# Optimization experiments

Hardware: AMD Instinct MI355X
Metric: run time of the kernel (lower is better)

Reference implementation:

```python
import jax, jax.numpy as jnp
import numpy as np

B, N, C, H = 1, 256, 128, 4
DH = C // H  # per-head dim = 32
KEY_SCALE = DH ** -0.5


def setup_inputs() -> dict:
    key = jax.random.key(0)
    ks = jax.random.split(key, 9)
    return {
        "q_data": jax.random.normal(ks[0], (B, N, N, C), jnp.float32),
        "m_data": jax.random.normal(ks[1], (B, N, N, C), jnp.float32),
        "bias": jax.random.normal(ks[2], (B, N, 1, 1, N), jnp.float32),
        "nonbatched_bias": jax.random.normal(ks[3], (1, H, N, N), jnp.float32),
        "wq": jax.random.normal(ks[4], (C, C), jnp.float32) * (1.0 / np.sqrt(C)),
        "wk": jax.random.normal(ks[5], (C, C), jnp.float32) * (1.0 / np.sqrt(C)),
        "wv": jax.random.normal(ks[6], (C, C), jnp.float32) * (1.0 / np.sqrt(C)),
        "wo": jax.random.normal(ks[7], (C, C), jnp.float32) * (1.0 / np.sqrt(C)),
        "bo": jnp.zeros((C,), jnp.float32),
        "wg": jax.random.normal(ks[8], (C, C), jnp.float32) * (1.0 / np.sqrt(C)),
        "bg": jnp.ones((C,), jnp.float32),
    }


def reference(q_data, m_data, bias, nonbatched_bias, wq, wk, wv, wo, bo, wg, bg):
    # projections (torch Linear: x @ W.T), weights stored [out, in]
    q = (q_data @ wq.T) * KEY_SCALE            # [B, N, Nq, H*DH]
    k = m_data @ wk.T                          # [B, N, Nk, H*DH]
    v = m_data @ wv.T                          # [B, N, Nk, H*DH]
    q = q.reshape(B, N, N, H, DH)
    k = k.reshape(B, N, N, H, DH)
    v = v.reshape(B, N, N, H, DH)
    # logits: [B, N, H, Nq, Nk]
    logits = jnp.einsum("bnqhd,bnkhd->bnhqk", q, k)
    logits = logits + bias + nonbatched_bias   # bias [B,N,1,1,Nk]; nb [1,H,Nq,Nk]
    weight = jax.nn.softmax(logits, axis=-1)
    wa = jnp.einsum("bnhqk,bnkhd->bnqhd", weight, v)  # [B, N, Nq, H, DH]
    g = jax.nn.sigmoid(q_data @ wg.T + bg).reshape(B, N, N, H, DH)
    wa = wa * g
    out = wa.reshape(B, N, N, H * DH) @ wo.T + bo
    return out
```

## Files before the change

### kernel.cpp

```cpp
#include <hip/hip_runtime.h>
#include <hip/hip_bf16.h>

typedef unsigned short u16;
typedef unsigned int u32;

#define N_ 256
#define C_ 128
#define H_ 4
#define DH_ 32
#define R_ (N_*N_)

static constexpr float KEY_SCALE_ = 0.17677669529663687f;

typedef __attribute__((ext_vector_type(8))) short bf16x8;
typedef __attribute__((ext_vector_type(4))) float f32x4;

__device__ __forceinline__ float bf2f(u16 b){ return __uint_as_float(((u32)b)<<16); }
__device__ __forceinline__ u16 f2bf(float f){
  u32 u = __float_as_uint(f);
  u += 0x7FFFu + ((u>>16)&1u);
  return (u16)(u>>16);
}

__global__ __launch_bounds__(256) void wconv_kernel(
    const float* __restrict__ wq, const float* __restrict__ wk,
    const float* __restrict__ wv, const float* __restrict__ wg,
    u16* __restrict__ wtb)
{
  int id = blockIdx.x*256 + threadIdx.x;
  int m = id >> 12;
  int e = (id & 4095)*4;
  const float* src = (m==0) ? wq : (m==1) ? wk : (m==2) ? wv : wg;
  const float4 v = *(const float4*)(src + e);
  const float s = (m==0) ? KEY_SCALE_ : 1.f;
  ushort4 o;
  o.x = f2bf(v.x*s); o.y = f2bf(v.y*s); o.z = f2bf(v.z*s); o.w = f2bf(v.w*s);
  *(ushort4*)(wtb + m*16384 + e) = o;
}

#define XSTR 136
__global__ __launch_bounds__(256, 2) void proj_kernel(
    const float* __restrict__ qd, const float* __restrict__ md,
    const u16* __restrict__ wtb, const float* __restrict__ bg,
    u16* __restrict__ qb, u16* __restrict__ kb,
    u16* __restrict__ vb, u16* __restrict__ gb)
{
  __shared__ u16 Xs[256*XSTR];
  const int t = threadIdx.x;
  const int y = blockIdx.y;
  const size_t row0 = (size_t)blockIdx.x * 256;
  const float* X = y ? md : qd;

  #pragma unroll
  for (int p=0;p<16;p++){
    int id = t + p*256;
    int r = id >> 4, c0 = (id & 15)*8;
    const float* s = X + (row0 + r)*C_ + c0;
    float4 a = *(const float4*)s;
    float4 b = *(const float4*)(s+4);
    u16* d = &Xs[r*XSTR + c0];
    d[0]=f2bf(a.x); d[1]=f2bf(a.y); d[2]=f2bf(a.z); d[3]=f2bf(a.w);
    d[4]=f2bf(b.x); d[5]=f2bf(b.y); d[6]=f2bf(b.z); d[7]=f2bf(b.w);
  }

  const int w = t >> 6, l = t & 63, c = l & 15, g = l >> 4;
  const int matSel = w >> 1;
  const int ctBase = (w & 1) * 4;
  const int matIdx = y ? (matSel ? 2 : 1) : (matSel ? 3 : 0);
  u16* dst = y ? (matSel ? vb : kb) : (matSel ? gb : qb);
  const bool doSig = (!y) && matSel;

  bf16x8 bfr[4][4];
  {
    const u16* wb = wtb + matIdx*16384;
    #pragma unroll
    for (int ctj=0;ctj<4;ctj++){
      const u16* rp = wb + ((ctBase+ctj)*16 + c)*C_ + g*8;
      #pragma unroll
      for (int kk=0;kk<4;kk++)
        bfr[ctj][kk] = *(const bf16x8*)(rp + kk*32);
    }
  }
  float bgv[4];
  if (doSig){
    #pragma unroll
    for (int ctj=0;ctj<4;ctj++) bgv[ctj] = bg[(ctBase+ctj)*16 + c];
  }
  __syncthreads();

  for (int mt=0; mt<16; mt++){
    bf16x8 af[4];
    #pragma unroll
    for (int kk=0;kk<4;kk++)
      af[kk] = *(const bf16x8*)&Xs[(mt*16 + c)*XSTR + kk*32 + g*8];
    f32x4 a0 = {0.f,0.f,0.f,0.f}, a1 = {0.f,0.f,0.f,0.f};
    f32x4 a2 = {0.f,0.f,0.f,0.f}, a3 = {0.f,0.f,0.f,0.f};
    #pragma unroll
    for (int kk=0;kk<4;kk++){
      a0 = __builtin_amdgcn_mfma_f32_16x16x32_bf16(af[kk], bfr[0][kk], a0, 0,0,0);
      a1 = __builtin_amdgcn_mfma_f32_16x16x32_bf16(af[kk], bfr[1][kk], a1, 0,0,0);
      a2 = __builtin_amdgcn_mfma_f32_16x16x32_bf16(af[kk], bfr[2][kk], a2, 0,0,0);
      a3 = __builtin_amdgcn_mfma_f32_16x16x32_bf16(af[kk], bfr[3][kk], a3, 0,0,0);
    }
    f32x4 accs[4] = {a0,a1,a2,a3};
    #pragma unroll
    for (int ctj=0;ctj<4;ctj++){
      #pragma unroll
      for (int r=0;r<4;r++){
        float v = accs[ctj][r];
        if (doSig) v = 1.f/(1.f+__expf(-(v + bgv[ctj])));
        dst[(row0 + mt*16 + 4*g + r)*C_ + (ctBase+ctj)*16 + c] = f2bf(v);
      }
    }
  }
}

#define VSTR 264
__global__ __launch_bounds__(256) void attn_kernel(
    const u16* qb, const u16* __restrict__ kb,
    const u16* __restrict__ vb, const u16* __restrict__ gb,
    const float* __restrict__ bias, const float* __restrict__ nbias,
    u16* wab)
{
  __shared__ u16 Vt[32*VSTR];
  __shared__ u16 Ps[4][16][VSTR];
  __shared__ float Bs[256];

  const int t  = threadIdx.x;
  const int h  = blockIdx.x;
  const int n  = blockIdx.y;
  const int w  = t >> 6;
  const int l  = t & 63;
  const int c  = l & 15;
  const int g  = l >> 4;

  {
    const u16* vsrc = vb + ((size_t)n*N_)*C_ + h*DH_;
    for (int id = t; id < 1024; id += 256){
      int k = id >> 2, ch = id & 3;
      ushort4 a = *(const ushort4*)(vsrc + (size_t)k*C_ + ch*8);
      ushort4 b = *(const ushort4*)(vsrc + (size_t)k*C_ + ch*8 + 4);
      int d0 = ch*8;
      Vt[(d0+0)*VSTR + k] = a.x;  Vt[(d0+1)*VSTR + k] = a.y;
      Vt[(d0+2)*VSTR + k] = a.z;  Vt[(d0+3)*VSTR + k] = a.w;
      Vt[(d0+4)*VSTR + k] = b.x;  Vt[(d0+5)*VSTR + k] = b.y;
      Vt[(d0+6)*VSTR + k] = b.z;  Vt[(d0+7)*VSTR + k] = b.w;
    }
    Bs[t] = bias[(size_t)n*N_ + t];
  }
  __syncthreads();

  bf16x8 kf[16];
  {
    const u16* kbase = kb + ((size_t)(n*N_ + c))*C_ + h*DH_ + g*8;
    #pragma unroll
    for (int kt=0;kt<16;kt++)
      kf[kt] = *(const bf16x8*)(kbase + (size_t)kt*16*C_);
  }

  const float* nbp = nbias + (size_t)h*N_*N_;

  for (int qt=0; qt<4; qt++){
    const int q0 = w*64 + qt*16;

    bf16x8 af = *(const bf16x8*)(qb + ((size_t)(n*N_ + q0 + c))*C_ + h*DH_ + g*8);

    const float* nbrow = nbp + (size_t)(q0 + 4*g)*N_ + c;
    f32x4 acc[16];
    #pragma unroll
    for (int kt=0;kt<16;kt++){
      const float bsv = Bs[kt*16 + c];
      f32x4 ci;
      #pragma unroll
      for (int r=0;r<4;r++) ci[r] = bsv + nbrow[(size_t)r*N_ + kt*16];
      acc[kt] = __builtin_amdgcn_mfma_f32_16x16x32_bf16(af, kf[kt], ci, 0, 0, 0);
    }

    float inv[4];
    #pragma unroll
    for (int r=0;r<4;r++){
      float m = acc[0][r];
      #pragma unroll
      for (int kt=1;kt<16;kt++) m = fmaxf(m, acc[kt][r]);
      #pragma unroll
      for (int s=8;s>=1;s>>=1) m = fmaxf(m, __shfl_xor(m, s));
      float sum = 0.f;
      #pragma unroll
      for (int kt=0;kt<16;kt++){
        float p = __expf(acc[kt][r] - m);
        acc[kt][r] = p;
        sum += p;
      }
      #pragma unroll
      for (int s=8;s>=1;s>>=1) sum += __shfl_xor(sum, s);
      inv[r] = 1.f/sum;
    }

    #pragma unroll
    for (int kt=0;kt<16;kt++){
      #pragma unroll
      for (int r=0;r<4;r++)
        Ps[w][4*g + r][kt*16 + c] = f2bf(acc[kt][r]);
    }

    f32x4 o0 = {0.f,0.f,0.f,0.f}, o1 = {0.f,0.f,0.f,0.f};
    #pragma unroll
    for (int s=0;s<8;s++){
      bf16x8 pa = *(const bf16x8*)&Ps[w][c][s*32 + g*8];
      bf16x8 v0 = *(const bf16x8*)&Vt[(size_t)c*VSTR      + s*32 + g*8];
      bf16x8 v1 = *(const bf16x8*)&Vt[(size_t)(16+c)*VSTR + s*32 + g*8];
      o0 = __builtin_amdgcn_mfma_f32_16x16x32_bf16(pa, v0, o0, 0, 0, 0);
      o1 = __builtin_amdgcn_mfma_f32_16x16x32_bf16(pa, v1, o1, 0, 0, 0);
    }

    #pragma unroll
    for (int r=0;r<4;r++){
      size_t row = (size_t)n*N_ + q0 + 4*g + r;
      float gv0 = bf2f(gb[row*C_ + h*DH_ + c]);
      float gv1 = bf2f(gb[row*C_ + h*DH_ + 16 + c]);
      wab[row*C_ + h*DH_ + c]      = f2bf(o0[r]*inv[r]*gv0);
      wab[row*C_ + h*DH_ + 16 + c] = f2bf(o1[r]*inv[r]*gv1);
    }
  }
}

#define WSTR 136
__global__ __launch_bounds__(256, 2) void outproj_kernel(
    const u16* __restrict__ wab, const float* __restrict__ wo,
    const float* __restrict__ bo, float* __restrict__ out)
{
  __shared__ u16 Wos[128*WSTR];
  const int t = threadIdx.x;
  const size_t row0 = (size_t)blockIdx.x * 128;

  #pragma unroll
  for (int p=0;p<8;p++){
    int id = t + p*256;
    int r = id >> 4, c0 = (id & 15)*8;
    const float* s = wo + r*C_ + c0;
    float4 a = *(const float4*)s;
    float4 b = *(const float4*)(s+4);
    u16* d = &Wos[r*WSTR + c0];
    d[0]=f2bf(a.x); d[1]=f2bf(a.y); d[2]=f2bf(a.z); d[3]=f2bf(a.w);
    d[4]=f2bf(b.x); d[5]=f2bf(b.y); d[6]=f2bf(b.z); d[7]=f2bf(b.w);
  }

  const int w = t >> 6, l = t & 63, c = l & 15, g = l >> 4;

  bf16x8 af[2][4];
  #pragma unroll
  for (int mt=0;mt<2;mt++){
    const u16* ap = wab + (row0 + w*32 + mt*16 + c)*C_ + g*8;
    #pragma unroll
    for (int kk=0;kk<4;kk++)
      af[mt][kk] = *(const bf16x8*)(ap + kk*32);
  }
  __syncthreads();

  for (int ct=0;ct<8;ct++){
    bf16x8 bfr[4];
    #pragma unroll
    for (int kk=0;kk<4;kk++)
      bfr[kk] = *(const bf16x8*)&Wos[(ct*16 + c)*WSTR + kk*32 + g*8];
    f32x4 acc0 = {0.f,0.f,0.f,0.f}, acc1 = {0.f,0.f,0.f,0.f};
    #pragma unroll
    for (int kk=0;kk<4;kk++){
      acc0 = __builtin_amdgcn_mfma_f32_16x16x32_bf16(af[0][kk], bfr[kk], acc0, 0,0,0);
      acc1 = __builtin_amdgcn_mfma_f32_16x16x32_bf16(af[1][kk], bfr[kk], acc1, 0,0,0);
    }
    const float bov = bo[ct*16 + c];
    #pragma unroll
    for (int r=0;r<4;r++){
      out[(row0 + w*32 +      4*g + r)*C_ + ct*16 + c] = acc0[r] + bov;
      out[(row0 + w*32 + 16 + 4*g + r)*C_ + ct*16 + c] = acc1[r] + bov;
    }
  }
}

extern "C" void kernel_launch(void* const* d_in, const int* in_sizes, int n_in,
                              void* d_out, int out_size, void* d_ws, size_t ws_size,
                              hipStream_t stream) {
  const float* qd   = (const float*)d_in[0];
  const float* md   = (const float*)d_in[1];
  const float* bias = (const float*)d_in[2];
  const float* nb   = (const float*)d_in[3];
  const float* wq   = (const float*)d_in[4];
  const float* wk   = (const float*)d_in[5];
  const float* wv   = (const float*)d_in[6];
  const float* wo   = (const float*)d_in[7];
  const float* bo   = (const float*)d_in[8];
  const float* wg   = (const float*)d_in[9];
  const float* bg   = (const float*)d_in[10];
  float* out = (float*)d_out;

  char* ws = (char*)d_ws;
  const size_t MB16 = (size_t)16*1024*1024;
  u16* qb  = (u16*)(ws);
  u16* kb  = (u16*)(ws + MB16);
  u16* vb  = (u16*)(ws + 2*MB16);
  u16* gb  = (u16*)(ws + 3*MB16);
  u16* wab = qb;
  u16* wtb = (u16*)d_out;

  wconv_kernel<<<64, 256, 0, stream>>>(wq, wk, wv, wg, wtb);
  proj_kernel<<<dim3(256, 2), 256, 0, stream>>>(qd, md, wtb, bg, qb, kb, vb, gb);
  attn_kernel<<<dim3(H_, N_), 256, 0, stream>>>(qb, kb, vb, gb, bias, nb, wab);
  outproj_kernel<<<512, 256, 0, stream>>>(wab, wo, bo, out);
}
```

Before: 120.8 us.

## Split attention blocks across query halves and shrink P staging buffer

Launches 2048 attention blocks (256 rows × 4 heads × 2 query halves) instead of 1024, with each wave handling 32 query rows, to raise occupancy and parallelism. The probability tile is staged in small double-buffered 16x32 LDS chunks per k-step instead of a full 16x256 row, which cuts LDS use. V rows are permuted (even/odd interleave) so gate loads and output stores become packed 32-bit accesses. The cost is that V and K are loaded and transposed twice per (n,h), and there is no barrier between waves, so correctness relies on each wave reusing only its own slice.

```diff
diff --git a/kernel.cpp b/kernel.cpp
--- a/kernel.cpp
+++ b/kernel.cpp
@@ -123,28 +123,36 @@
     u16* wab)
 {
   __shared__ u16 Vt[32*VSTR];
-  __shared__ u16 Ps[4][16][VSTR];
+  __shared__ u16 Ps0[4][16][36];
+  __shared__ u16 Ps1[4][16][36];
   __shared__ float Bs[256];
 
-  const int t  = threadIdx.x;
-  const int h  = blockIdx.x;
-  const int n  = blockIdx.y;
-  const int w  = t >> 6;
-  const int l  = t & 63;
-  const int c  = l & 15;
-  const int g  = l >> 4;
+  const int t   = threadIdx.x;
+  const int id  = blockIdx.x;
+  const int n   = id & 255;
+  const int sub = id >> 8;
+  const int h   = sub & 3;
+  const int qh  = sub >> 2;
+  const int w   = t >> 6;
+  const int l   = t & 63;
+  const int c   = l & 15;
+  const int g   = l >> 4;
 
   {
     const u16* vsrc = vb + ((size_t)n*N_)*C_ + h*DH_;
-    for (int id = t; id < 1024; id += 256){
-      int k = id >> 2, ch = id & 3;
+    for (int idx = t; idx < 1024; idx += 256){
+      int k = idx >> 2, ch = idx & 3;
       ushort4 a = *(const ushort4*)(vsrc + (size_t)k*C_ + ch*8);
       ushort4 b = *(const ushort4*)(vsrc + (size_t)k*C_ + ch*8 + 4);
+      u16 e[8] = {(u16)a.x,(u16)a.y,(u16)a.z,(u16)a.w,
+                  (u16)b.x,(u16)b.y,(u16)b.z,(u16)b.w};
       int d0 = ch*8;
-      Vt[(d0+0)*VSTR + k] = a.x;  Vt[(d0+1)*VSTR + k] = a.y;
-      Vt[(d0+2)*VSTR + k] = a.z;  Vt[(d0+3)*VSTR + k] = a.w;
-      Vt[(d0+4)*VSTR + k] = b.x;  Vt[(d0+5)*VSTR + k] = b.y;
-      Vt[(d0+6)*VSTR + k] = b.z;  Vt[(d0+7)*VSTR + k] = b.w;
+      #pragma unroll
+      for (int jj=0;jj<8;jj++){
+        int d = d0 + jj;
+        int vr = (d&1)*16 + (d>>1);
+        Vt[vr*VSTR + k] = e[jj];
+      }
     }
     Bs[t] = bias[(size_t)n*N_ + t];
   }
@@ -160,8 +168,8 @@
 
   const float* nbp = nbias + (size_t)h*N_*N_;
 
-  for (int qt=0; qt<4; qt++){
-    const int q0 = w*64 + qt*16;
+  for (int qt=0; qt<2; qt++){
+    const int q0 = qh*128 + w*32 + qt*16;
 
     bf16x8 af = *(const bf16x8*)(qb + ((size_t)(n*N_ + q0 + c))*C_ + h*DH_ + g*8);
 
@@ -196,17 +204,16 @@
       inv[r] = 1.f/sum;
     }
 
-    #pragma unroll
-    for (int kt=0;kt<16;kt++){
-      #pragma unroll
-      for (int r=0;r<4;r++)
-        Ps[w][4*g + r][kt*16 + c] = f2bf(acc[kt][r]);
-    }
-
     f32x4 o0 = {0.f,0.f,0.f,0.f}, o1 = {0.f,0.f,0.f,0.f};
     #pragma unroll
     for (int s=0;s<8;s++){
-      bf16x8 pa = *(const bf16x8*)&Ps[w][c][s*32 + g*8];
+      u16 (*Psb)[16][36] = (s&1) ? Ps1 : Ps0;
+      #pragma unroll
+      for (int r=0;r<4;r++){
+        Psb[w][4*g+r][c]      = f2bf(acc[2*s  ][r]);
+        Psb[w][4*g+r][16 + c] = f2bf(acc[2*s+1][r]);
+      }
+      bf16x8 pa = *(const bf16x8*)&Psb[w][c][g*8];
       bf16x8 v0 = *(const bf16x8*)&Vt[(size_t)c*VSTR      + s*32 + g*8];
       bf16x8 v1 = *(const bf16x8*)&Vt[(size_t)(16+c)*VSTR + s*32 + g*8];
       o0 = __builtin_amdgcn_mfma_f32_16x16x32_bf16(pa, v0, o0, 0, 0, 0);
@@ -216,10 +223,11 @@
     #pragma unroll
     for (int r=0;r<4;r++){
       size_t row = (size_t)n*N_ + q0 + 4*g + r;
-      float gv0 = bf2f(gb[row*C_ + h*DH_ + c]);
-      float gv1 = bf2f(gb[row*C_ + h*DH_ + 16 + c]);
-      wab[row*C_ + h*DH_ + c]      = f2bf(o0[r]*inv[r]*gv0);
-      wab[row*C_ + h*DH_ + 16 + c] = f2bf(o1[r]*inv[r]*gv1);
+      u32 g2 = *(const u32*)&gb[row*C_ + h*DH_ + 2*c];
+      float g0v = bf2f((u16)(g2 & 0xFFFFu));
+      float g1v = bf2f((u16)(g2 >> 16));
+      u32 ov = (u32)f2bf(o0[r]*inv[r]*g0v) | ((u32)f2bf(o1[r]*inv[r]*g1v) << 16);
+      *(u32*)&wab[row*C_ + h*DH_ + 2*c] = ov;
     }
   }
 }
@@ -304,6 +312,6 @@
 
   wconv_kernel<<<64, 256, 0, stream>>>(wq, wk, wv, wg, wtb);
   proj_kernel<<<dim3(256, 2), 256, 0, stream>>>(qd, md, wtb, bg, qb, kb, vb, gb);
-  attn_kernel<<<dim3(H_, N_), 256, 0, stream>>>(qb, kb, vb, gb, bias, nb, wab);
+  attn_kernel<<<2048, 256, 0, stream>>>(qb, kb, vb, gb, bias, nb, wab);
   outproj_kernel<<<512, 256, 0, stream>>>(wab, wo, bo, out);
 }
```

New measurement: 191.1 us. 1.58x slower.

## Pre-transpose nonbatched bias and permute P/V key order for vectorized accesses

Applied to the files above, without the earlier changes.

Adds a small kernel that transposes the per-head nonbatched bias into a scratch area of the output buffer. The attention kernel can then load four consecutive query-row bias values with one float4 instead of four strided scalar loads. The key dimension of V in shared memory is permuted to match a new packed layout for the probability matrix, so P is written as two bf16 values per 32-bit store instead of scalar 16-bit stores. This costs one extra launch and an extra pass over the 1 MB bias, and reuses output memory as temporary storage.

```diff
diff --git a/kernel.cpp b/kernel.cpp
--- a/kernel.cpp
+++ b/kernel.cpp
@@ -20,6 +20,9 @@
   u32 u = __float_as_uint(f);
   u += 0x7FFFu + ((u>>16)&1u);
   return (u16)(u>>16);
+}
+__device__ __forceinline__ u32 pack2bf(float lo, float hi){
+  return (u32)f2bf(lo) | ((u32)f2bf(hi) << 16);
 }
 
 __global__ __launch_bounds__(256) void wconv_kernel(
@@ -38,6 +41,30 @@
   *(ushort4*)(wtb + m*16384 + e) = o;
 }
 
+__global__ __launch_bounds__(256) void nbtr_kernel(
+    const float* __restrict__ nb, float* __restrict__ nbT)
+{
+  __shared__ float T[64][65];
+  const int t = threadIdx.x;
+  const int q0 = (blockIdx.x & 3)*64, k0 = (blockIdx.x >> 2)*64;
+  const int h = blockIdx.y;
+  const float* src = nb + (size_t)h*N_*N_;
+  float* dst = nbT + (size_t)h*N_*N_;
+  #pragma unroll
+  for (int p=0;p<16;p++){
+    int id = t + p*256;
+    int r = id >> 6, cc = id & 63;
+    T[cc][r] = src[(size_t)(q0 + r)*N_ + k0 + cc];
+  }
+  __syncthreads();
+  #pragma unroll
+  for (int p=0;p<16;p++){
+    int id = t + p*256;
+    int r = id >> 6, cc = id & 63;
+    dst[(size_t)(k0 + r)*N_ + q0 + cc] = T[r][cc];
+  }
+}
+
 #define XSTR 136
 __global__ __launch_bounds__(256, 2) void proj_kernel(
     const float* __restrict__ qd, const float* __restrict__ md,
@@ -119,7 +146,7 @@
 __global__ __launch_bounds__(256) void attn_kernel(
     const u16* qb, const u16* __restrict__ kb,
     const u16* __restrict__ vb, const u16* __restrict__ gb,
-    const float* __restrict__ bias, const float* __restrict__ nbias,
+    const float* __restrict__ bias, const float* __restrict__ nbT,
     u16* wab)
 {
   __shared__ u16 Vt[32*VSTR];
@@ -136,15 +163,16 @@
 
   {
     const u16* vsrc = vb + ((size_t)n*N_)*C_ + h*DH_;
-    for (int id = t; id < 1024; id += 256){
-      int k = id >> 2, ch = id & 3;
+    for (int idx = t; idx < 1024; idx += 256){
+      int k = idx >> 2, ch = idx & 3;
+      int sk = (k & ~31) | ((k & 15) << 1) | ((k >> 4) & 1);
       ushort4 a = *(const ushort4*)(vsrc + (size_t)k*C_ + ch*8);
       ushort4 b = *(const ushort4*)(vsrc + (size_t)k*C_ + ch*8 + 4);
       int d0 = ch*8;
-      Vt[(d0+0)*VSTR + k] = a.x;  Vt[(d0+1)*VSTR + k] = a.y;
-      Vt[(d0+2)*VSTR + k] = a.z;  Vt[(d0+3)*VSTR + k] = a.w;
-      Vt[(d0+4)*VSTR + k] = b.x;  Vt[(d0+5)*VSTR + k] = b.y;
-      Vt[(d0+6)*VSTR + k] = b.z;  Vt[(d0+7)*VSTR + k] = b.w;
+      Vt[(d0+0)*VSTR + sk] = a.x;  Vt[(d0+1)*VSTR + sk] = a.y;
+      Vt[(d0+2)*VSTR + sk] = a.z;  Vt[(d0+3)*VSTR + sk] = a.w;
+      Vt[(d0+4)*VSTR + sk] = b.x;  Vt[(d0+5)*VSTR + sk] = b.y;
+      Vt[(d0+6)*VSTR + sk] = b.z;  Vt[(d0+7)*VSTR + sk] = b.w;
     }
     Bs[t] = bias[(size_t)n*N_ + t];
   }
@@ -158,21 +186,21 @@
       kf[kt] = *(const bf16x8*)(kbase + (size_t)kt*16*C_);
   }
 
-  const float* nbp = nbias + (size_t)h*N_*N_;
+  const float* nbtp = nbT + (size_t)h*N_*N_;
 
   for (int qt=0; qt<4; qt++){
     const int q0 = w*64 + qt*16;
 
     bf16x8 af = *(const bf16x8*)(qb + ((size_t)(n*N_ + q0 + c))*C_ + h*DH_ + g*8);
 
-    const float* nbrow = nbp + (size_t)(q0 + 4*g)*N_ + c;
     f32x4 acc[16];
     #pragma unroll
     for (int kt=0;kt<16;kt++){
       const float bsv = Bs[kt*16 + c];
+      const float4 nb4 = *(const float4*)(nbtp + (size_t)(kt*16 + c)*N_ + q0 + 4*g);
       f32x4 ci;
-      #pragma unroll
-      for (int r=0;r<4;r++) ci[r] = bsv + nbrow[(size_t)r*N_ + kt*16];
+      ci[0] = bsv + nb4.x; ci[1] = bsv + nb4.y;
+      ci[2] = bsv + nb4.z; ci[3] = bsv + nb4.w;
       acc[kt] = __builtin_amdgcn_mfma_f32_16x16x32_bf16(af, kf[kt], ci, 0, 0, 0);
     }
 
@@ -197,10 +225,10 @@
     }
 
     #pragma unroll
-    for (int kt=0;kt<16;kt++){
+    for (int m=0;m<8;m++){
       #pragma unroll
       for (int r=0;r<4;r++)
-        Ps[w][4*g + r][kt*16 + c] = f2bf(acc[kt][r]);
+        *(u32*)&Ps[w][4*g+r][32*m + 2*c] = pack2bf(acc[2*m][r], acc[2*m+1][r]);
     }
 
     f32x4 o0 = {0.f,0.f,0.f,0.f}, o1 = {0.f,0.f,0.f,0.f};
@@ -300,10 +328,12 @@
   u16* vb  = (u16*)(ws + 2*MB16);
   u16* gb  = (u16*)(ws + 3*MB16);
   u16* wab = qb;
-  u16* wtb = (u16*)d_out;
+  u16*   wtb = (u16*)d_out;
+  float* nbT = (float*)((char*)d_out + 131072);
 
   wconv_kernel<<<64, 256, 0, stream>>>(wq, wk, wv, wg, wtb);
+  nbtr_kernel<<<dim3(16, 4), 256, 0, stream>>>(nb, nbT);
   proj_kernel<<<dim3(256, 2), 256, 0, stream>>>(qd, md, wtb, bg, qb, kb, vb, gb);
-  attn_kernel<<<dim3(H_, N_), 256, 0, stream>>>(qb, kb, vb, gb, bias, nb, wab);
+  attn_kernel<<<dim3(H_, N_), 256, 0, stream>>>(qb, kb, vb, gb, bias, nbT, wab);
   outproj_kernel<<<512, 256, 0, stream>>>(wab, wo, bo, out);
 }
```

New measurement: 135.1 us. +11.8%, slower.
